# Kernel optimization log

Measured on AMD Instinct MI355X. Metric: run time of the kernel, lower is better.

Reference implementation:

```python
import jax, jax.numpy as jnp
import numpy as np

B, L, W = 4, 512, 256
VOCAB, E, H = 30000, 300, 768
N_LABELS = 6


def setup_inputs() -> dict:
    key = jax.random.key(0)
    ks = jax.random.split(key, 7)
    return {
        "word_seq": jax.random.randint(ks[0], (B, W), 0, VOCAB),
        "hidden_state": jax.random.normal(ks[1], (B, L, H), dtype=jnp.float32),
        "label_value_matrix": jax.random.randint(ks[2], (B, L, W), 0, N_LABELS),
        "emb_a": jax.random.normal(ks[3], (VOCAB, E), dtype=jnp.float32) * 0.02,
        "lin_w": jax.random.normal(ks[4], (E, H), dtype=jnp.float32) * 0.02,
        "lin_b": jax.random.normal(ks[5], (H,), dtype=jnp.float32) * 0.02,
        "emb_c": jax.random.normal(ks[6], (N_LABELS, H), dtype=jnp.float32) * 0.02,
    }


def reference(word_seq, hidden_state, label_value_matrix, emb_a, lin_w, lin_b, emb_c):
    temper = jnp.asarray(emb_c.shape[1], hidden_state.dtype) ** 0.5  # hidden_size ** 0.5
    # embedding_a lookup + linear projection: [B,W,E] -> [B,W,H]
    a = emb_a[word_seq] @ lin_w + lin_b
    # attention-style scores u = hidden_state @ a^T / temper : [B,L,W]
    u = jnp.einsum("blh,bwh->blw", hidden_state, a) / temper
    # masked exp-normalize WITHOUT max-subtraction (faithful to original)
    mask = jnp.clip(label_value_matrix, 0, 1).astype(u.dtype)
    delta_exp_u = jnp.exp(u) * mask
    p = delta_exp_u / (jnp.sum(delta_exp_u, axis=2, keepdims=True) + 1e-10)
    # embedding_c gather [B,L,W,H], weight by p and reduce over W -> [B,L,H]
    ec = emb_c[label_value_matrix]
    o = jnp.einsum("blw,blwh->blh", p, ec)
    return o
```

## Files before the change

kernel.cpp:

```cpp
#include <hip/hip_runtime.h>

#define BB 4
#define LL 512
#define WW 256
#define EE 300
#define HH 768

typedef __attribute__((ext_vector_type(8))) short bf16x8;
typedef __attribute__((ext_vector_type(4))) float f32x4;

__device__ __forceinline__ short f2bf(float f) {
    union { float f; unsigned u; } v; v.f = f;
    unsigned r = (v.u + 0x7FFFu + ((v.u >> 16) & 1u)) >> 16;
    return (short)r;
}

__global__ __launch_bounds__(256, 1) void kA_a_gemm(
    const int*   __restrict__ word_seq,
    const float* __restrict__ emb_a,
    const float* __restrict__ lin_w,
    const float* __restrict__ lin_b,
    short*       __restrict__ aT)
{
    __shared__ short eaL[2][64 * 168];
    __shared__ short lwL[2][64 * 168];

    const int t  = threadIdx.x;
    const int m0 = (blockIdx.x & 15) * 64;
    const int n0 = (blockIdx.x >> 4) * 64;

    const int lane = t & 63, wv = t >> 6;
    const int l15 = lane & 15, l4 = lane >> 4;

    const int r_ea = t >> 2;
    const int q_ea = t & 3;
    const int h_lw = t & 63;
    const int q_lw = t >> 6;

    const int    wrow = word_seq[m0 + r_ea];
    const float* arow = emb_a + (long)wrow * EE;

    f32x4 acc[4] = {};
    float ea_reg[40], lw_reg[40];

#pragma unroll
    for (int half = 0; half < 2; ++half) {
        const int k0 = half * 160;
        {
            const int cbase = k0 + q_ea * 40;
#pragma unroll
            for (int c4 = 0; c4 < 10; ++c4) {
                const int col = cbase + c4 * 4;
                if (col <= 296) {
                    const float4 p = *(const float4*)(arow + col);
                    ea_reg[c4 * 4 + 0] = p.x; ea_reg[c4 * 4 + 1] = p.y;
                    ea_reg[c4 * 4 + 2] = p.z; ea_reg[c4 * 4 + 3] = p.w;
                } else {
                    ea_reg[c4 * 4 + 0] = 0.f; ea_reg[c4 * 4 + 1] = 0.f;
                    ea_reg[c4 * 4 + 2] = 0.f; ea_reg[c4 * 4 + 3] = 0.f;
                }
            }
            const int cb2 = k0 + q_lw * 40;
#pragma unroll
            for (int j = 0; j < 40; ++j) {
                const int col = cb2 + j;
                lw_reg[j] = (col < EE) ? lin_w[(long)col * HH + n0 + h_lw] : 0.f;
            }
        }
        {
            const int eoff = r_ea * 168 + q_ea * 40;
#pragma unroll
            for (int c8 = 0; c8 < 5; ++c8) {
                bf16x8 sv;
#pragma unroll
                for (int j = 0; j < 8; ++j) sv[j] = f2bf(ea_reg[c8 * 8 + j]);
                *(bf16x8*)(&eaL[half][eoff + c8 * 8]) = sv;
            }
            const int loff = h_lw * 168 + q_lw * 40;
#pragma unroll
            for (int c8 = 0; c8 < 5; ++c8) {
                bf16x8 sv;
#pragma unroll
                for (int j = 0; j < 8; ++j) sv[j] = f2bf(lw_reg[c8 * 8 + j]);
                *(bf16x8*)(&lwL[half][loff + c8 * 8]) = sv;
            }
        }
        __syncthreads();
#pragma unroll
        for (int ks = 0; ks < 5; ++ks) {
            const bf16x8 af =
                *(const bf16x8*)(&eaL[half][(wv * 16 + l15) * 168 + ks * 32 + l4 * 8]);
#pragma unroll
            for (int nf = 0; nf < 4; ++nf) {
                const bf16x8 bfv =
                    *(const bf16x8*)(&lwL[half][(nf * 16 + l15) * 168 + ks * 32 + l4 * 8]);
                acc[nf] = __builtin_amdgcn_mfma_f32_16x16x32_bf16(af, bfv, acc[nf], 0, 0, 0);
            }
        }
    }

    const int b1 = m0 >> 8;
#pragma unroll
    for (int nf = 0; nf < 4; ++nf) {
        const int h    = n0 + nf * 16 + l15;
        const float bv = lin_b[h];
        const long hbase = ((long)(b1 * 96 + (h >> 3)) * 256) * 8 + (h & 7);
#pragma unroll
        for (int i = 0; i < 4; ++i) {
            const int w = (m0 & 255) + wv * 16 + l4 * 4 + i;
            aT[hbase + (long)w * 8] = f2bf(acc[nf][i] + bv);
        }
    }
}

__global__ __launch_bounds__(512) void kB_attn_out(
    const float* __restrict__ hidden,
    const int*   __restrict__ label,
    const short* __restrict__ aT,
    const float* __restrict__ emb_c,
    float*       __restrict__ out)
{
    __shared__ short hid[16 * 776];
    __shared__ float s_lds[8][16][5];
    __shared__ float s_fin[8][5];
    __shared__ float invd[8];

    const int t = threadIdx.x, lane = t & 63, wv = t >> 6;
    const int l15 = lane & 15, l4 = lane >> 4;
    const int row0 = blockIdx.x * 8;
    const int b    = row0 >> 9;

    {
        const float* hrow = hidden + (long)row0 * HH;
        const bf16x8 z = {};
#pragma unroll
        for (int j = 0; j < 2; ++j) {
            const int ci = t + j * 512;
            if (ci < 768) {
                const int row = ci / 96;
                const int col = (ci - row * 96) * 8;
                const float4 p0 = *(const float4*)(hrow + (long)row * HH + col);
                const float4 p1 = *(const float4*)(hrow + (long)row * HH + col + 4);
                bf16x8 v;
                v[0] = f2bf(p0.x); v[1] = f2bf(p0.y); v[2] = f2bf(p0.z); v[3] = f2bf(p0.w);
                v[4] = f2bf(p1.x); v[5] = f2bf(p1.y); v[6] = f2bf(p1.z); v[7] = f2bf(p1.w);
                *(bf16x8*)(&hid[row * 776 + col]) = v;
                *(bf16x8*)(&hid[(8 + row) * 776 + col]) = z;
            }
        }
    }

    int lv[2][4];
#pragma unroll
    for (int nf = 0; nf < 2; ++nf) {
        const int w = wv * 32 + nf * 16 + l15;
#pragma unroll
        for (int i = 0; i < 4; ++i) {
            const int row = l4 * 4 + i;
            lv[nf][i] = (row < 8) ? label[((long)row0 + row) * WW + w] : 0;
        }
    }
    __syncthreads();

    const short* abase = aT + (long)b * 96 * 256 * 8;
    f32x4 acc[2] = {};
#pragma unroll
    for (int ks = 0; ks < 24; ++ks) {
        const bf16x8 af = *(const bf16x8*)(&hid[l15 * 776 + ks * 32 + l4 * 8]);
#pragma unroll
        for (int nf = 0; nf < 2; ++nf) {
            const int w = wv * 32 + nf * 16 + l15;
            const bf16x8 bfv =
                *(const bf16x8*)(abase + ((long)(ks * 4 + l4) * 256 + w) * 8);
            acc[nf] = __builtin_amdgcn_mfma_f32_16x16x32_bf16(af, bfv, acc[nf], 0, 0, 0);
        }
    }

    const float inv_temper = 0.03608439182435161f;
    float s_loc[4][5];
#pragma unroll
    for (int i = 0; i < 4; ++i)
#pragma unroll
        for (int c = 0; c < 5; ++c) s_loc[i][c] = 0.f;
#pragma unroll
    for (int nf = 0; nf < 2; ++nf) {
#pragma unroll
        for (int i = 0; i < 4; ++i) {
            const float e = __expf(acc[nf][i] * inv_temper);
#pragma unroll
            for (int c = 1; c <= 5; ++c)
                s_loc[i][c - 1] += (lv[nf][i] == c) ? e : 0.f;
        }
    }
#pragma unroll
    for (int i = 0; i < 4; ++i) {
#pragma unroll
        for (int c = 0; c < 5; ++c) {
            float v = s_loc[i][c];
            v += __shfl_xor(v, 1);
            v += __shfl_xor(v, 2);
            v += __shfl_xor(v, 4);
            v += __shfl_xor(v, 8);
            s_loc[i][c] = v;
        }
    }
    if (l15 == 0) {
#pragma unroll
        for (int i = 0; i < 4; ++i)
#pragma unroll
            for (int c = 0; c < 5; ++c)
                s_lds[wv][l4 * 4 + i][c] = s_loc[i][c];
    }
    __syncthreads();
    if (t < 8) {
        float den = 1e-10f;
#pragma unroll
        for (int c = 0; c < 5; ++c) {
            float s = 0.f;
#pragma unroll
            for (int q = 0; q < 8; ++q) s += s_lds[q][t][c];
            s_fin[t][c] = s;
            den += s;
        }
        invd[t] = 1.0f / den;
    }
    __syncthreads();

    float ecv0[5], ecv1[5];
#pragma unroll
    for (int c = 0; c < 5; ++c) {
        ecv0[c] = emb_c[(c + 1) * HH + t];
        ecv1[c] = (t < 256) ? emb_c[(c + 1) * HH + 512 + t] : 0.f;
    }

    float* obase = out + (long)row0 * HH;
#pragma unroll
    for (int r = 0; r < 8; ++r) {
        const float id = invd[r];
        const float s0 = s_fin[r][0], s1 = s_fin[r][1], s2 = s_fin[r][2],
                    s3 = s_fin[r][3], s4 = s_fin[r][4];
        {
            const float v = s0 * ecv0[0] + s1 * ecv0[1] + s2 * ecv0[2] +
                            s3 * ecv0[3] + s4 * ecv0[4];
            obase[(long)r * HH + t] = v * id;
        }
        if (t < 256) {
            const float v = s0 * ecv1[0] + s1 * ecv1[1] + s2 * ecv1[2] +
                            s3 * ecv1[3] + s4 * ecv1[4];
            obase[(long)r * HH + 512 + t] = v * id;
        }
    }
}

extern "C" void kernel_launch(void* const* d_in, const int* in_sizes, int n_in,
                              void* d_out, int out_size, void* d_ws, size_t ws_size,
                              hipStream_t stream) {
    const int*   word_seq = (const int*)  d_in[0];
    const float* hidden   = (const float*)d_in[1];
    const int*   label    = (const int*)  d_in[2];
    const float* emb_a    = (const float*)d_in[3];
    const float* lin_w    = (const float*)d_in[4];
    const float* lin_b    = (const float*)d_in[5];
    const float* emb_c    = (const float*)d_in[6];
    float* out = (float*)d_out;

    short* aT = (short*)d_ws;

    kA_a_gemm<<<dim3(192), 256, 0, stream>>>(word_seq, emb_a, lin_w, lin_b, aT);
    kB_attn_out<<<dim3(256), 512, 0, stream>>>(hidden, label, aT, emb_c, out);
}
```

Before: 24.33 us.

## Process 32 rows per block in attention kernel with XCD-aware batch mapping

Each block of the second kernel now handles 32 query rows instead of 8 (previously padded to 16 with zeros), using two M-fragments so every aT B-fragment load feeds two MFMAs. The grid shrinks from 256 to 64 blocks, and block indices are remapped so blocks on the same XCD share a batch, which improves L2 reuse of aT. In exchange only 64 CUs are used, so parallelism and latency hiding drop, and each block now does a longer serial output loop.

Measured after the change: 30.75 us. +26.4%, slower.

```diff
diff --git a/kernel.cpp b/kernel.cpp
--- a/kernel.cpp
+++ b/kernel.cpp
@@ -113,112 +113,122 @@
     }
 }
 
-__global__ __launch_bounds__(512) void kB_attn_out(
+__global__ __launch_bounds__(512, 1) void kB_attn_out(
     const float* __restrict__ hidden,
     const int*   __restrict__ label,
     const short* __restrict__ aT,
     const float* __restrict__ emb_c,
     float*       __restrict__ out)
 {
-    __shared__ short hid[16 * 776];
-    __shared__ float s_lds[8][16][5];
-    __shared__ float s_fin[8][5];
-    __shared__ float invd[8];
+    __shared__ short hid[32 * 776];
+    __shared__ float s_lds[8][2][16][5];
+    __shared__ float s_fin[32][5];
+    __shared__ float invd[32];
 
     const int t = threadIdx.x, lane = t & 63, wv = t >> 6;
     const int l15 = lane & 15, l4 = lane >> 4;
-    const int row0 = blockIdx.x * 8;
-    const int b    = row0 >> 9;
+
+    const int i_hw = blockIdx.x;
+    const int xcd  = i_hw & 7;
+    const int b    = xcd >> 1;
+    const int j    = ((xcd & 1) << 3) | (i_hw >> 3);
+    const int row0 = b * 512 + j * 32;
 
     {
         const float* hrow = hidden + (long)row0 * HH;
-        const bf16x8 z = {};
-#pragma unroll
-        for (int j = 0; j < 2; ++j) {
-            const int ci = t + j * 512;
-            if (ci < 768) {
-                const int row = ci / 96;
-                const int col = (ci - row * 96) * 8;
-                const float4 p0 = *(const float4*)(hrow + (long)row * HH + col);
-                const float4 p1 = *(const float4*)(hrow + (long)row * HH + col + 4);
-                bf16x8 v;
-                v[0] = f2bf(p0.x); v[1] = f2bf(p0.y); v[2] = f2bf(p0.z); v[3] = f2bf(p0.w);
-                v[4] = f2bf(p1.x); v[5] = f2bf(p1.y); v[6] = f2bf(p1.z); v[7] = f2bf(p1.w);
-                *(bf16x8*)(&hid[row * 776 + col]) = v;
-                *(bf16x8*)(&hid[(8 + row) * 776 + col]) = z;
-            }
-        }
-    }
-
-    int lv[2][4];
+#pragma unroll
+        for (int jj = 0; jj < 6; ++jj) {
+            const int ci  = t + jj * 512;
+            const int row = ci / 96;
+            const int col = (ci - row * 96) * 8;
+            const float4 p0 = *(const float4*)(hrow + (long)row * HH + col);
+            const float4 p1 = *(const float4*)(hrow + (long)row * HH + col + 4);
+            bf16x8 v;
+            v[0] = f2bf(p0.x); v[1] = f2bf(p0.y); v[2] = f2bf(p0.z); v[3] = f2bf(p0.w);
+            v[4] = f2bf(p1.x); v[5] = f2bf(p1.y); v[6] = f2bf(p1.z); v[7] = f2bf(p1.w);
+            *(bf16x8*)(&hid[row * 776 + col]) = v;
+        }
+    }
+
+    int lv[2][2][4];
 #pragma unroll
     for (int nf = 0; nf < 2; ++nf) {
         const int w = wv * 32 + nf * 16 + l15;
 #pragma unroll
-        for (int i = 0; i < 4; ++i) {
-            const int row = l4 * 4 + i;
-            lv[nf][i] = (row < 8) ? label[((long)row0 + row) * WW + w] : 0;
-        }
+        for (int mf = 0; mf < 2; ++mf)
+#pragma unroll
+            for (int i = 0; i < 4; ++i) {
+                const int row = mf * 16 + l4 * 4 + i;
+                lv[nf][mf][i] = label[((long)row0 + row) * WW + w];
+            }
     }
     __syncthreads();
 
     const short* abase = aT + (long)b * 96 * 256 * 8;
-    f32x4 acc[2] = {};
+    f32x4 acc[2][2] = {};
 #pragma unroll
     for (int ks = 0; ks < 24; ++ks) {
-        const bf16x8 af = *(const bf16x8*)(&hid[l15 * 776 + ks * 32 + l4 * 8]);
+        const bf16x8 af0 = *(const bf16x8*)(&hid[l15 * 776 + ks * 32 + l4 * 8]);
+        const bf16x8 af1 = *(const bf16x8*)(&hid[(16 + l15) * 776 + ks * 32 + l4 * 8]);
 #pragma unroll
         for (int nf = 0; nf < 2; ++nf) {
             const int w = wv * 32 + nf * 16 + l15;
             const bf16x8 bfv =
                 *(const bf16x8*)(abase + ((long)(ks * 4 + l4) * 256 + w) * 8);
-            acc[nf] = __builtin_amdgcn_mfma_f32_16x16x32_bf16(af, bfv, acc[nf], 0, 0, 0);
+            acc[0][nf] = __builtin_amdgcn_mfma_f32_16x16x32_bf16(af0, bfv, acc[0][nf], 0, 0, 0);
+            acc[1][nf] = __builtin_amdgcn_mfma_f32_16x16x32_bf16(af1, bfv, acc[1][nf], 0, 0, 0);
         }
     }
 
     const float inv_temper = 0.03608439182435161f;
-    float s_loc[4][5];
-#pragma unroll
-    for (int i = 0; i < 4; ++i)
-#pragma unroll
-        for (int c = 0; c < 5; ++c) s_loc[i][c] = 0.f;
-#pragma unroll
-    for (int nf = 0; nf < 2; ++nf) {
-#pragma unroll
-        for (int i = 0; i < 4; ++i) {
-            const float e = __expf(acc[nf][i] * inv_temper);
-#pragma unroll
-            for (int c = 1; c <= 5; ++c)
-                s_loc[i][c - 1] += (lv[nf][i] == c) ? e : 0.f;
-        }
-    }
-#pragma unroll
-    for (int i = 0; i < 4; ++i) {
-#pragma unroll
-        for (int c = 0; c < 5; ++c) {
-            float v = s_loc[i][c];
-            v += __shfl_xor(v, 1);
-            v += __shfl_xor(v, 2);
-            v += __shfl_xor(v, 4);
-            v += __shfl_xor(v, 8);
-            s_loc[i][c] = v;
-        }
-    }
+    float s_loc[2][4][5];
+#pragma unroll
+    for (int mf = 0; mf < 2; ++mf)
+#pragma unroll
+        for (int i = 0; i < 4; ++i)
+#pragma unroll
+            for (int c = 0; c < 5; ++c) s_loc[mf][i][c] = 0.f;
+#pragma unroll
+    for (int nf = 0; nf < 2; ++nf)
+#pragma unroll
+        for (int mf = 0; mf < 2; ++mf)
+#pragma unroll
+            for (int i = 0; i < 4; ++i) {
+                const float e = __expf(acc[mf][nf][i] * inv_temper);
+#pragma unroll
+                for (int c = 1; c <= 5; ++c)
+                    s_loc[mf][i][c - 1] += (lv[nf][mf][i] == c) ? e : 0.f;
+            }
+#pragma unroll
+    for (int mf = 0; mf < 2; ++mf)
+#pragma unroll
+        for (int i = 0; i < 4; ++i)
+#pragma unroll
+            for (int c = 0; c < 5; ++c) {
+                float v = s_loc[mf][i][c];
+                v += __shfl_xor(v, 1);
+                v += __shfl_xor(v, 2);
+                v += __shfl_xor(v, 4);
+                v += __shfl_xor(v, 8);
+                s_loc[mf][i][c] = v;
+            }
     if (l15 == 0) {
 #pragma unroll
-        for (int i = 0; i < 4; ++i)
-#pragma unroll
-            for (int c = 0; c < 5; ++c)
-                s_lds[wv][l4 * 4 + i][c] = s_loc[i][c];
+        for (int mf = 0; mf < 2; ++mf)
+#pragma unroll
+            for (int i = 0; i < 4; ++i)
+#pragma unroll
+                for (int c = 0; c < 5; ++c)
+                    s_lds[wv][mf][l4 * 4 + i][c] = s_loc[mf][i][c];
     }
     __syncthreads();
-    if (t < 8) {
+    if (t < 32) {
         float den = 1e-10f;
 #pragma unroll
         for (int c = 0; c < 5; ++c) {
             float s = 0.f;
 #pragma unroll
-            for (int q = 0; q < 8; ++q) s += s_lds[q][t][c];
+            for (int q = 0; q < 8; ++q) s += s_lds[q][t >> 4][t & 15][c];
             s_fin[t][c] = s;
             den += s;
         }
@@ -235,7 +245,7 @@
 
     float* obase = out + (long)row0 * HH;
 #pragma unroll
-    for (int r = 0; r < 8; ++r) {
+    for (int r = 0; r < 32; ++r) {
         const float id = invd[r];
         const float s0 = s_fin[r][0], s1 = s_fin[r][1], s2 = s_fin[r][2],
                     s3 = s_fin[r][3], s4 = s_fin[r][4];
@@ -267,5 +277,5 @@
     short* aT = (short*)d_ws;
 
     kA_a_gemm<<<dim3(192), 256, 0, stream>>>(word_seq, emb_a, lin_w, lin_b, aT);
-    kB_attn_out<<<dim3(256), 512, 0, stream>>>(hidden, label, aT, emb_c, out);
-}
+    kB_attn_out<<<dim3(64), 512, 0, stream>>>(hidden, label, aT, emb_c, out);
+}
```
